# Kernel tuning notes

Measured on AMD Instinct MI355X. Metric: run time of the kernel, lower is better.

Reference implementation:

```python
import jax, jax.numpy as jnp
import numpy as np

N_HEAD = 16
ROPE_BASE = 10000.0


def apply_rope(x):
    # x: [B, T, H, D], torchtune interleaved-pair RoPE
    B, T, H, D = x.shape
    pos = jnp.arange(T, dtype=jnp.float32)
    freqs = 1.0 / (ROPE_BASE ** (jnp.arange(0, D, 2, dtype=jnp.float32) / D))  # [D/2]
    theta = pos[:, None] * freqs[None, :]            # [T, D/2]
    cos = jnp.cos(theta)[None, :, None, :]           # [1, T, 1, D/2]
    sin = jnp.sin(theta)[None, :, None, :]
    xp = x.reshape(B, T, H, D // 2, 2)
    x0, x1 = xp[..., 0], xp[..., 1]
    out = jnp.stack([x0 * cos - x1 * sin, x1 * cos + x0 * sin], axis=-1)
    return out.reshape(B, T, H, D).astype(x.dtype)


def setup_inputs() -> dict:
    key = jax.random.key(0)
    k1, k2, k3 = jax.random.split(key, 3)
    B, T, C = 4, 2048, 1024
    x = jax.random.normal(k1, (B, T, C), dtype=jnp.float32)
    w_qkv = jax.random.normal(k2, (C, 3 * C), dtype=jnp.float32) * 0.02
    b_qkv = jnp.zeros((3 * C,), dtype=jnp.float32)
    w_proj = jax.random.normal(k3, (C, C), dtype=jnp.float32) * 0.02
    b_proj = jnp.zeros((C,), dtype=jnp.float32)
    return {"x": x, "w_qkv": w_qkv, "b_qkv": b_qkv, "w_proj": w_proj, "b_proj": b_proj}


def reference(x, w_qkv, b_qkv, w_proj, b_proj):
    B, T, C = x.shape
    H = N_HEAD
    D = C // H
    qkv = x @ w_qkv + b_qkv                          # [B, T, 3C]
    q, k, v = jnp.split(qkv, 3, axis=-1)
    q = apply_rope(q.reshape(B, T, H, D))
    k = apply_rope(k.reshape(B, T, H, D))
    v = v.reshape(B, T, H, D)
    scale = 1.0 / jnp.sqrt(jnp.asarray(D, dtype=x.dtype))
    attn = jnp.einsum('bthd,bshd->bhts', q, k) * scale  # [B, H, T, T] (non-causal)
    attn = jax.nn.softmax(attn, axis=-1)
    out = jnp.einsum('bhts,bshd->bthd', attn, v).reshape(B, T, C)
    return out @ w_proj + b_proj
```

## Files before the change

kernel.cpp:

```cpp
#include <hip/hip_runtime.h>

typedef unsigned short ushort_t;
typedef unsigned int   uint_t;
typedef __attribute__((ext_vector_type(8))) short bf16x8;
typedef __attribute__((ext_vector_type(4))) float f32x4;

__device__ __forceinline__ ushort_t f2bf(float f) {
    union { float f; uint_t i; } x; x.f = f;
    uint_t i = x.i + 0x7fffu + ((x.i >> 16) & 1u);
    return (ushort_t)(i >> 16);
}
__device__ __forceinline__ uint_t fbits(float f) {
    union { float f; uint_t i; } x; x.f = f;
    return x.i;
}
__device__ __forceinline__ void async16(const void* g, void* l) {
    __builtin_amdgcn_global_load_lds(
        (const __attribute__((address_space(1))) uint_t*)g,
        (__attribute__((address_space(3))) uint_t*)l, 16, 0, 0);
}

__global__ __launch_bounds__(256) void conv_bf16(
    const float* __restrict__ in, ushort_t* __restrict__ outp)
{
    int i = (blockIdx.x * 256 + threadIdx.x) * 4;
    float4 v = *(const float4*)(in + i);
    uint_t a = (uint_t)f2bf(v.x) | ((uint_t)f2bf(v.y) << 16);
    uint_t b = (uint_t)f2bf(v.z) | ((uint_t)f2bf(v.w) << 16);
    uint2 st = { a, b };
    *(uint2*)(outp + i) = st;
}

__global__ __launch_bounds__(256) void transpose_conv(
    const float* __restrict__ in, ushort_t* __restrict__ outp, int R, int C)
{
    __shared__ ushort_t t[64][65];
    int r0 = blockIdx.y * 64, c0 = blockIdx.x * 64;
    int lr = threadIdx.x >> 4, lc = (threadIdx.x & 15) * 4;
#pragma unroll
    for (int rr = 0; rr < 4; ++rr) {
        float4 v = *(const float4*)(in + (size_t)(r0 + rr * 16 + lr) * C + c0 + lc);
        t[lc + 0][rr * 16 + lr] = f2bf(v.x);
        t[lc + 1][rr * 16 + lr] = f2bf(v.y);
        t[lc + 2][rr * 16 + lr] = f2bf(v.z);
        t[lc + 3][rr * 16 + lr] = f2bf(v.w);
    }
    __syncthreads();
    int oc = threadIdx.x >> 2, och = (threadIdx.x & 3) * 16;
    union { uint4 v[2]; ushort_t u[16]; } pk;
#pragma unroll
    for (int j = 0; j < 16; ++j) pk.u[j] = t[oc][och + j];
    uint4* dst = (uint4*)(outp + (size_t)(c0 + oc) * R + r0 + och);
    dst[0] = pk.v[0]; dst[1] = pk.v[1];
}

__global__ __launch_bounds__(256) void rope_table_k(float2* __restrict__ tab)
{
    int idx = blockIdx.x * 256 + threadIdx.x;
    int t = idx >> 5, i = idx & 31;
    float freq = powf(10000.0f, -(float)i * (1.0f / 32.0f));
    float sn, cs;
    sincosf((float)t * freq, &sn, &cs);
    tab[idx] = make_float2(cs, sn);
}

template <int MODE>
__global__ __launch_bounds__(256) void gemm_mfma(
    const ushort_t* __restrict__ A, const ushort_t* __restrict__ Bt,
    const float* __restrict__ bias, void* __restrict__ Cv,
    const float2* __restrict__ tab, int M, int N, int K, int coloff)
{
    __shared__ ushort_t As[128][64];
    __shared__ ushort_t Bs[128][64];
    const int tid = threadIdx.x;
    const int w = tid >> 6, lane = tid & 63, ln = lane & 15, quad = lane >> 4;
    const int wm = w >> 1, wn = w & 1;

    const int lin = blockIdx.y * gridDim.x + blockIdx.x;
    const int per = (gridDim.x * gridDim.y) >> 3;
    const int nid = (lin & 7) * per + (lin >> 3);
    const int bx = nid % gridDim.x, by = nid / gridDim.x;
    const int row0 = by * 128, col0 = bx * 128 + coloff;

    f32x4 acc[4][4] = {};

    const int swch = (lane & 7) ^ (lane >> 3);
    const ushort_t* ga = A  + (size_t)(row0 + w * 8 + (lane >> 3)) * K + swch * 8;
    const ushort_t* gb = Bt + (size_t)(col0 + w * 8 + (lane >> 3)) * K + swch * 8;
    ushort_t* la = &As[w * 8][0];
    ushort_t* lb = &Bs[w * 8][0];
    const int rch0 = ln & 7;

    for (int k0 = 0; k0 < K; k0 += 64) {
#pragma unroll
        for (int j = 0; j < 4; ++j) {
            async16(ga + (size_t)(j * 32) * K + k0, la + j * 32 * 64);
            async16(gb + (size_t)(j * 32) * K + k0, lb + j * 32 * 64);
        }
        __syncthreads();
#pragma unroll
        for (int kk = 0; kk < 2; ++kk) {
            int ch = ((kk * 4 + quad) ^ rch0) * 8;
            bf16x8 af[4], bfv[4];
#pragma unroll
            for (int mt = 0; mt < 4; ++mt)
                af[mt] = *(const bf16x8*)&As[wm * 64 + mt * 16 + ln][ch];
#pragma unroll
            for (int nt = 0; nt < 4; ++nt)
                bfv[nt] = *(const bf16x8*)&Bs[wn * 64 + nt * 16 + ln][ch];
#pragma unroll
            for (int mt = 0; mt < 4; ++mt)
#pragma unroll
                for (int nt = 0; nt < 4; ++nt) {
                    if (MODE == 2)
                        acc[mt][nt] = __builtin_amdgcn_mfma_f32_16x16x32_bf16(
                            af[mt], bfv[nt], acc[mt][nt], 0, 0, 0);
                    else
                        acc[mt][nt] = __builtin_amdgcn_mfma_f32_16x16x32_bf16(
                            bfv[nt], af[mt], acc[mt][nt], 0, 0, 0);
                }
        }
        __syncthreads();
    }

    if (MODE == 2) {
#pragma unroll
        for (int nt = 0; nt < 4; ++nt) {
            int c = col0 + wn * 64 + nt * 16 + ln;
            float bv = bias[c];
            int c2 = c - 2048;
            size_t vrow = ((size_t)(c2 >> 6)) * 64 + (c2 & 63);
#pragma unroll
            for (int mt = 0; mt < 4; ++mt) {
                int rr = row0 + wm * 64 + mt * 16 + quad * 4;
                int b = rr >> 11, t0 = rr & 2047;
                uint2 st;
                st.x = (uint_t)f2bf(acc[mt][nt][0] + bv)
                     | ((uint_t)f2bf(acc[mt][nt][1] + bv) << 16);
                st.y = (uint_t)f2bf(acc[mt][nt][2] + bv)
                     | ((uint_t)f2bf(acc[mt][nt][3] + bv) << 16);
                *(uint2*)((ushort_t*)Cv + ((size_t)b * 16 * 64 + vrow) * 2048 + t0) = st;
            }
        }
    } else {
#pragma unroll
        for (int mt = 0; mt < 4; ++mt) {
            int rr = row0 + wm * 64 + mt * 16 + ln;
#pragma unroll
            for (int nt = 0; nt < 4; ++nt) {
                int c0 = col0 + wn * 64 + nt * 16 + quad * 4;
                float4 bv = *(const float4*)(bias + c0);
                float v0 = acc[mt][nt][0] + bv.x, v1 = acc[mt][nt][1] + bv.y;
                float v2 = acc[mt][nt][2] + bv.z, v3 = acc[mt][nt][3] + bv.w;
                if (MODE == 1) {
                    int i0 = (c0 & 63) >> 1;
                    const float2* trow = tab + (size_t)(rr & 2047) * 32;
                    float2 cs0 = trow[i0], cs1 = trow[i0 + 1];
                    float o0 = v0 * cs0.x - v1 * cs0.y;
                    float o1 = v1 * cs0.x + v0 * cs0.y;
                    float o2 = v2 * cs1.x - v3 * cs1.y;
                    float o3 = v3 * cs1.x + v2 * cs1.y;
                    uint2 st;
                    st.x = (uint_t)f2bf(o0) | ((uint_t)f2bf(o1) << 16);
                    st.y = (uint_t)f2bf(o2) | ((uint_t)f2bf(o3) << 16);
                    *(uint2*)((ushort_t*)Cv + (size_t)rr * N + c0) = st;
                } else {
                    float4 st = { v0, v1, v2, v3 };
                    *(float4*)((float*)Cv + (size_t)rr * N + c0) = st;
                }
            }
        }
    }
}

__global__ __launch_bounds__(512, 4) void attn_mfma(
    const ushort_t* __restrict__ qkv, const ushort_t* __restrict__ vtg,
    ushort_t* __restrict__ outp)
{
    __shared__ ushort_t Ks[2][64][64];
    __shared__ ushort_t Vts[2][64][64];
    __shared__ ushort_t Ps[8][16][72];

    const int tid = threadIdx.x;
    const int w = tid >> 6, lane = tid & 63, ln = lane & 15, quad = lane >> 4;
    const int bh = blockIdx.x, qt = blockIdx.y, b = bh >> 4, h = bh & 15;
    const size_t base = (size_t)b * 2048 * 3072 + h * 64;

    bf16x8 af[2][2];
#pragma unroll
    for (int s = 0; s < 2; ++s)
#pragma unroll
        for (int kk = 0; kk < 2; ++kk)
            af[s][kk] = *(const bf16x8*)(qkv + base
                + (size_t)(qt * 256 + w * 32 + s * 16 + ln) * 3072 + kk * 32 + quad * 8);

    bf16x8 ones;
#pragma unroll
    for (int j = 0; j < 8; ++j) ones[j] = (short)0x3F80;

    f32x4 oaccT[2][4] = {};
    f32x4 oneacc[2] = {};
    const float SC = 0.125f * 1.44269504f;

    const int swch = (lane & 7) ^ (lane >> 3);
    const ushort_t* kg = qkv + base + 1024 + (size_t)(lane >> 3) * 3072 + swch * 8;
    const ushort_t* vg = vtg + ((size_t)bh * 64 + (lane >> 3)) * 2048 + swch * 8;
    const int rch0 = ln & 7;
    const int r8 = w * 8;

    async16(kg + (size_t)r8 * 3072, &Ks[0][r8][0]);
    async16(vg + (size_t)r8 * 2048, &Vts[0][r8][0]);
    asm volatile("s_waitcnt vmcnt(0)" ::: "memory");
    __builtin_amdgcn_s_barrier();

    int cur = 0;
    for (int kt = 0; kt < 32; ++kt) {
        if (kt < 31) {
            async16(kg + (size_t)((kt + 1) * 64 + r8) * 3072, &Ks[cur ^ 1][r8][0]);
            async16(vg + (size_t)r8 * 2048 + (kt + 1) * 64, &Vts[cur ^ 1][r8][0]);
        }

        bf16x8 kf[2][4], vf[2][4];
#pragma unroll
        for (int kk = 0; kk < 2; ++kk) {
            int ch = ((kk * 4 + quad) ^ rch0) * 8;
#pragma unroll
            for (int nt = 0; nt < 4; ++nt) {
                kf[kk][nt] = *(const bf16x8*)&Ks[cur][nt * 16 + ln][ch];
                vf[kk][nt] = *(const bf16x8*)&Vts[cur][nt * 16 + ln][ch];
            }
        }

#pragma unroll
        for (int s = 0; s < 2; ++s) {
            f32x4 sacc[4] = {};
#pragma unroll
            for (int kk = 0; kk < 2; ++kk)
#pragma unroll
                for (int nt = 0; nt < 4; ++nt)
                    sacc[nt] = __builtin_amdgcn_mfma_f32_16x16x32_bf16(
                        kf[kk][nt], af[s][kk], sacc[nt], 0, 0, 0);

            if (s == 1)
                asm volatile("s_waitcnt lgkmcnt(0)" ::: "memory");
#pragma unroll
            for (int nt = 0; nt < 4; ++nt) {
                float e0 = __builtin_amdgcn_exp2f(fmaf(sacc[nt][0], SC, -24.0f));
                float e1 = __builtin_amdgcn_exp2f(fmaf(sacc[nt][1], SC, -24.0f));
                float e2 = __builtin_amdgcn_exp2f(fmaf(sacc[nt][2], SC, -24.0f));
                float e3 = __builtin_amdgcn_exp2f(fmaf(sacc[nt][3], SC, -24.0f));
                uint2 pk;
                pk.x = __builtin_amdgcn_perm(fbits(e1), fbits(e0), 0x07060302u);
                pk.y = __builtin_amdgcn_perm(fbits(e3), fbits(e2), 0x07060302u);
                *(uint2*)&Ps[w][ln][nt * 16 + quad * 4] = pk;
            }
            asm volatile("s_waitcnt lgkmcnt(0)" ::: "memory");

#pragma unroll
            for (int kk = 0; kk < 2; ++kk) {
                bf16x8 pf = *(const bf16x8*)&Ps[w][ln][kk * 32 + quad * 8];
                oneacc[s] = __builtin_amdgcn_mfma_f32_16x16x32_bf16(
                    ones, pf, oneacc[s], 0, 0, 0);
#pragma unroll
                for (int nt = 0; nt < 4; ++nt)
                    oaccT[s][nt] = __builtin_amdgcn_mfma_f32_16x16x32_bf16(
                        vf[kk][nt], pf, oaccT[s][nt], 0, 0, 0);
            }
        }

        asm volatile("s_waitcnt vmcnt(0) lgkmcnt(0)" ::: "memory");
        __builtin_amdgcn_s_barrier();
        cur ^= 1;
    }

#pragma unroll
    for (int s = 0; s < 2; ++s) {
        float linv = 1.0f / oneacc[s][0];
        size_t row = (size_t)b * 2048 + qt * 256 + w * 32 + s * 16 + ln;
#pragma unroll
        for (int nt = 0; nt < 4; ++nt) {
            uint2 st;
            st.x = (uint_t)f2bf(oaccT[s][nt][0] * linv)
                 | ((uint_t)f2bf(oaccT[s][nt][1] * linv) << 16);
            st.y = (uint_t)f2bf(oaccT[s][nt][2] * linv)
                 | ((uint_t)f2bf(oaccT[s][nt][3] * linv) << 16);
            *(uint2*)(outp + row * 1024 + h * 64 + nt * 16 + quad * 4) = st;
        }
    }
}

extern "C" void kernel_launch(void* const* d_in, const int* in_sizes, int n_in,
                              void* d_out, int out_size, void* d_ws, size_t ws_size,
                              hipStream_t stream)
{
    (void)in_sizes; (void)n_in; (void)out_size; (void)ws_size;

    const float* x      = (const float*)d_in[0];
    const float* w_qkv  = (const float*)d_in[1];
    const float* b_qkv  = (const float*)d_in[2];
    const float* w_proj = (const float*)d_in[3];
    const float* b_proj = (const float*)d_in[4];
    float*       out    = (float*)d_out;

    ushort_t* x_bf    = (ushort_t*)d_ws;
    ushort_t* wqkvT   = x_bf    + (size_t)8192 * 1024;
    ushort_t* wprojT  = wqkvT   + (size_t)3072 * 1024;
    ushort_t* qkv_bf  = wprojT  + (size_t)1024 * 1024;
    ushort_t* attn_bf = qkv_bf  + (size_t)8192 * 3072;
    ushort_t* vtg     = attn_bf + (size_t)8192 * 1024;
    float2*   tab     = (float2*)(vtg + (size_t)64 * 64 * 2048);

    conv_bf16<<<8192, 256, 0, stream>>>(x, x_bf);
    transpose_conv<<<dim3(48, 16), 256, 0, stream>>>(w_qkv, wqkvT, 1024, 3072);
    transpose_conv<<<dim3(16, 16), 256, 0, stream>>>(w_proj, wprojT, 1024, 1024);
    rope_table_k<<<256, 256, 0, stream>>>(tab);

    gemm_mfma<1><<<dim3(16, 64), 256, 0, stream>>>(
        x_bf, wqkvT, b_qkv, qkv_bf, tab, 8192, 3072, 1024, 0);

    gemm_mfma<2><<<dim3(8, 64), 256, 0, stream>>>(
        x_bf, wqkvT, b_qkv, vtg, nullptr, 8192, 3072, 1024, 2048);

    attn_mfma<<<dim3(64, 8), 512, 0, stream>>>(qkv_bf, vtg, attn_bf);

    gemm_mfma<0><<<dim3(8, 64), 256, 0, stream>>>(
        attn_bf, wprojT, b_proj, out, nullptr, 8192, 1024, 1024, 0);
}
```

Baseline: 289.0 us.

## Use dedicated 256x256-tile GEMM with fused RoPE for Q/K projection

Replaces the generic MFMA GEMM for the Q/K part of the QKV projection with a specialized kernel using 256x256 output tiles, 512 threads, double-buffered async global-to-LDS loads with XOR swizzle, and a grouped block-index remap for L2 locality. Bias add and RoPE stay fused in the epilogue, which writes bf16. Larger tiles raise arithmetic intensity and cut global traffic, but they also mean more registers, 128 KB of LDS per block, and fewer blocks (256) to fill the GPU.

```diff
diff --git a/kernel.cpp b/kernel.cpp
--- a/kernel.cpp
+++ b/kernel.cpp
@@ -173,6 +173,103 @@
     }
 }
 
+__global__ __launch_bounds__(512, 2) void gemm256_rope(
+    const ushort_t* __restrict__ A, const ushort_t* __restrict__ Bt,
+    const float* __restrict__ bias, ushort_t* __restrict__ C,
+    const float2* __restrict__ tab)
+{
+    __shared__ ushort_t As[2][256][64];
+    __shared__ ushort_t Bs[2][256][64];
+
+    const int tid = threadIdx.x;
+    const int w = tid >> 6, lane = tid & 63, ln = lane & 15, quad = lane >> 4;
+    const int wm = w >> 2, wn = w & 3;
+
+    const int lin = blockIdx.y * 8 + blockIdx.x;
+    const int nid = (lin & 7) * 32 + (lin >> 3);
+    const int bx = nid & 7, by = nid >> 3;
+    const int row0 = by * 256, col0 = bx * 256;
+
+    const int r6 = tid >> 3, c8 = tid & 7;
+    const int swch = c8 ^ (r6 & 7);
+    const ushort_t* ga = A  + (size_t)(row0 + r6) * 1024 + swch * 8;
+    const ushort_t* gb = Bt + (size_t)(col0 + r6) * 1024 + swch * 8;
+    ushort_t* lau = &As[0][0][0] + tid * 8;
+    ushort_t* lbu = &Bs[0][0][0] + tid * 8;
+    const int rch0 = ln & 7;
+
+    f32x4 acc[8][4] = {};
+
+#pragma unroll
+    for (int j = 0; j < 4; ++j) {
+        async16(ga + (size_t)(j * 64) * 1024, lau + j * 4096);
+        async16(gb + (size_t)(j * 64) * 1024, lbu + j * 4096);
+    }
+    asm volatile("s_waitcnt vmcnt(0)" ::: "memory");
+    __builtin_amdgcn_s_barrier();
+
+#pragma unroll 2
+    for (int k = 0; k < 16; ++k) {
+        const int cur = k & 1;
+        const int kn = (k < 15) ? k + 1 : k;
+        const size_t koff = (size_t)kn * 64;
+#pragma unroll
+        for (int j = 0; j < 4; ++j) {
+            async16(ga + (size_t)(j * 64) * 1024 + koff, lau + (cur ^ 1) * 16384 + j * 4096);
+            async16(gb + (size_t)(j * 64) * 1024 + koff, lbu + (cur ^ 1) * 16384 + j * 4096);
+        }
+        bf16x8 bf[4];
+#pragma unroll
+        for (int q = 0; q < 4; ++q) {
+            const int kk = q >> 1, mh = q & 1;
+            const int ch = ((kk * 4 + quad) ^ rch0) * 8;
+            if (mh == 0) {
+#pragma unroll
+                for (int nt = 0; nt < 4; ++nt)
+                    bf[nt] = *(const bf16x8*)&Bs[cur][wn * 64 + nt * 16 + ln][ch];
+            }
+            bf16x8 af[4];
+#pragma unroll
+            for (int mt = 0; mt < 4; ++mt)
+                af[mt] = *(const bf16x8*)&As[cur][mh * 128 + wm * 64 + mt * 16 + ln][ch];
+            __builtin_amdgcn_s_setprio(1);
+#pragma unroll
+            for (int mt = 0; mt < 4; ++mt)
+#pragma unroll
+                for (int nt = 0; nt < 4; ++nt)
+                    acc[mh * 4 + mt][nt] = __builtin_amdgcn_mfma_f32_16x16x32_bf16(
+                        bf[nt], af[mt], acc[mh * 4 + mt][nt], 0, 0, 0);
+            __builtin_amdgcn_s_setprio(0);
+            if (q == 3)
+                asm volatile("s_waitcnt vmcnt(0)" ::: "memory");
+            __builtin_amdgcn_s_barrier();
+        }
+    }
+
+#pragma unroll
+    for (int mg = 0; mg < 8; ++mg) {
+        const int rr = row0 + (mg >> 2) * 128 + wm * 64 + (mg & 3) * 16 + ln;
+        const float2* trow = tab + (size_t)(rr & 2047) * 32;
+#pragma unroll
+        for (int nt = 0; nt < 4; ++nt) {
+            const int c0 = col0 + wn * 64 + nt * 16 + quad * 4;
+            float4 bv = *(const float4*)(bias + c0);
+            float v0 = acc[mg][nt][0] + bv.x, v1 = acc[mg][nt][1] + bv.y;
+            float v2 = acc[mg][nt][2] + bv.z, v3 = acc[mg][nt][3] + bv.w;
+            const int i0 = (c0 & 63) >> 1;
+            float2 cs0 = trow[i0], cs1 = trow[i0 + 1];
+            float o0 = v0 * cs0.x - v1 * cs0.y;
+            float o1 = v1 * cs0.x + v0 * cs0.y;
+            float o2 = v2 * cs1.x - v3 * cs1.y;
+            float o3 = v3 * cs1.x + v2 * cs1.y;
+            uint2 st;
+            st.x = (uint_t)f2bf(o0) | ((uint_t)f2bf(o1) << 16);
+            st.y = (uint_t)f2bf(o2) | ((uint_t)f2bf(o3) << 16);
+            *(uint2*)(C + (size_t)rr * 3072 + c0) = st;
+        }
+    }
+}
+
 __global__ __launch_bounds__(512, 4) void attn_mfma(
     const ushort_t* __restrict__ qkv, const ushort_t* __restrict__ vtg,
     ushort_t* __restrict__ outp)
@@ -315,8 +412,7 @@
     transpose_conv<<<dim3(16, 16), 256, 0, stream>>>(w_proj, wprojT, 1024, 1024);
     rope_table_k<<<256, 256, 0, stream>>>(tab);
 
-    gemm_mfma<1><<<dim3(16, 64), 256, 0, stream>>>(
-        x_bf, wqkvT, b_qkv, qkv_bf, tab, 8192, 3072, 1024, 0);
+    gemm256_rope<<<dim3(8, 32), 512, 0, stream>>>(x_bf, wqkvT, b_qkv, qkv_bf, tab);
 
     gemm_mfma<2><<<dim3(8, 64), 256, 0, stream>>>(
         x_bf, wqkvT, b_qkv, vtg, nullptr, 8192, 3072, 1024, 2048);
```

Result: faster. 279.9 us (-3.2%).
